# Kernel tuning notes

Hardware: AMD Instinct MI355X
Metric: run time of the kernel (lower is better)

The kernel has to match this reference:

```python
import jax, jax.numpy as jnp
import numpy as np

B, H, S, W, F = 16, 4, 8, 256, 16


def setup_inputs() -> dict:
    key = jax.random.key(0)
    kx, kk = jax.random.split(key)
    x = jax.random.normal(kx, (B, S, W, F), dtype=jnp.float32)
    kernel = jax.random.normal(kk, (H, S, S, W), dtype=jnp.float32)
    return {"x": x, "kernel": kernel}


def reference(x, kernel):
    # kernel: [H, S, S, W]; x: [B, S, W, F]
    Hh, Ss, _, Ww = kernel.shape
    r = jnp.arange(Ww)
    # stacked[h,x,y,j,i] = roll(kernel, shifts=j+1)[i] = kernel[(i-(j+1)) % W]
    idx = (r[None, :] - (r[:, None] + 1)) % Ww          # [W(row=j), W(col=i)]
    stacked = kernel[..., idx]                            # [H,S,S,W,W]
    # torch.tril over last two dims: keep col i <= row j
    tri = (r[None, :] <= r[:, None])                      # [W,W]
    stacked = jnp.where(tri, stacked, jnp.zeros((), dtype=stacked.dtype))
    # masked triangular time-mix contraction
    out = jnp.einsum('hxyji,bxif->bhxyjf', stacked, x)    # [B,H,S,S,W,F]
    base = jnp.arange(1, Ww + 1, dtype=out.dtype).reshape(1, 1, 1, 1, Ww, 1)
    out = out / base
    # transform_x: on diagonal series (x==y) roll time dim by 1, zero first step
    diag_mod = jnp.roll(out, 1, axis=4)
    not_first = (r != 0).reshape(1, 1, 1, 1, Ww, 1)
    diag_mod = diag_mod * not_first.astype(out.dtype)
    eye = jnp.eye(Ss, dtype=bool).reshape(1, 1, Ss, Ss, 1, 1)
    return jnp.where(eye, diag_mod, out)
```

## Files before the change

kernel.cpp:

```cpp
#include <hip/hip_runtime.h>
#include <hip/hip_bf16.h>

typedef short short8 __attribute__((ext_vector_type(8)));
typedef float f32x4 __attribute__((ext_vector_type(4)));

union FragAB { int i[4]; short8 v; };

constexpr int Wc = 256, Fc = 16, Hc = 4, Sc = 8;

__global__ __launch_bounds__(256)
void k_fused(const float* __restrict__ x,
             const float* __restrict__ kern,
             float* __restrict__ out)
{
    __shared__ __align__(16) ushort Xts[128 * 264];
    __shared__ float wext2[2][576];
    __shared__ float rtab[2][256];

    const int blk = blockIdx.x;
    const int c  = blk & 15;
    const int nt = (blk >> 4) & 1;
    const int mt = (blk >> 5) & 1;
    const int sx = blk >> 6;
    const int t = threadIdx.x;

    rtab[0][t] = 1.0f / (float)(t + 1);
    rtab[1][t] = (t > 0) ? 1.0f / (float)t : 0.0f;

    #pragma unroll
    for (int e2 = 0; e2 < 2; ++e2) {
        int hy = c * 2 + e2;
        int h = hy >> 3, sy = hy & 7;
        const float* krow = kern + ((h * Sc + sx) * Sc + sy) * Wc;
        #pragma unroll
        for (int q = 0; q < 3; ++q) {
            int idx = q * 256 + t;
            if (idx < 576) wext2[e2][idx] = (idx >= 320) ? krow[575 - idx] : 0.0f;
        }
    }

    {
        const float4* xbase = reinterpret_cast<const float4*>(x);
        const int b0 = nt * 8;
        #pragma unroll
        for (int it = 0; it < 16; ++it) {
            int id = it * 256 + t;
            int fq = id & 3;
            int k2 = (id >> 2) & 127;
            int bl = id >> 9;
            const float4* rowp = xbase + ((size_t)((b0 + bl) * 8 + sx)) * 1024;
            float4 a = rowp[(2 * k2) * 4 + fq];
            float4 cq = rowp[(2 * k2 + 1) * 4 + fq];
            #pragma unroll
            for (int e = 0; e < 4; ++e) {
                float va = (&a.x)[e], vb = (&cq.x)[e];
                __hip_bfloat16 ha = __float2bfloat16(va);
                __hip_bfloat16 hb = __float2bfloat16(vb);
                uint u = (uint)reinterpret_cast<ushort&>(ha) |
                         ((uint)reinterpret_cast<ushort&>(hb) << 16);
                int row = bl * 16 + fq * 4 + e;
                *reinterpret_cast<uint*>(reinterpret_cast<char*>(Xts) + row * 528 + k2 * 4) = u;
            }
        }
    }
    __syncthreads();

    const int lane = t & 63, wid = t >> 6;
    const int wr = wid >> 1, wc = wid & 1;
    const int wm0 = mt * 128 + wr * 64;
    const int laneM = lane & 15, laneG = lane >> 4;

    const char* bbase = reinterpret_cast<const char*>(Xts) + (wc * 64 + laneM) * 528 + laneG * 16;
    const int kmax = (wm0 + 64 < 256) ? (wm0 + 64) : 256;

    #pragma unroll
    for (int e2 = 0; e2 < 2; ++e2) {
        int hy = c * 2 + e2;
        int h = hy >> 3, sy = hy & 7;
        const int diag = (sx == sy) ? 1 : 0;
        const float* wextf = wext2[e2];
        const float* rt = rtab[diag];
        const int abase = (320 - diag) + wm0 + laneM - 8 * laneG;

        f32x4 zero = {0.0f, 0.0f, 0.0f, 0.0f};
        f32x4 acc[4][4];
        #pragma unroll
        for (int m = 0; m < 4; ++m)
            #pragma unroll
            for (int n = 0; n < 4; ++n) acc[m][n] = zero;

        for (int kc = 0; kc < kmax; kc += 32) {
            FragAB bf[4];
            #pragma unroll
            for (int n = 0; n < 4; ++n) {
                int4 raw = *reinterpret_cast<const int4*>(bbase + n * (16 * 528) + kc * 2);
                bf[n].i[0] = raw.x; bf[n].i[1] = raw.y; bf[n].i[2] = raw.z; bf[n].i[3] = raw.w;
            }
            FragAB af[4];
            #pragma unroll
            for (int m = 0; m < 4; ++m) {
                int idx0 = abase + 16 * m - kc;
                float v[8];
                #pragma unroll
                for (int e = 0; e < 8; ++e) v[e] = wextf[idx0 - e];
                #pragma unroll
                for (int r = 0; r < 4; ++r)
                    af[m].i[r] = (int)__builtin_amdgcn_perm(__float_as_uint(v[2 * r + 1]),
                                                            __float_as_uint(v[2 * r]),
                                                            0x07060302u);
            }
            #pragma unroll
            for (int m = 0; m < 4; ++m)
                #pragma unroll
                for (int n = 0; n < 4; ++n)
                    acc[m][n] = __builtin_amdgcn_mfma_f32_16x16x32_bf16(af[m].v, bf[n].v,
                                                                        acc[m][n], 0, 0, 0);
        }

        #pragma unroll
        for (int n = 0; n < 4; ++n) {
            int b_ = nt * 8 + wc * 4 + n;
            float* ob = out + ((((((size_t)b_ * Hc + h) * Sc + sx) * Sc + sy) * Wc)) * Fc + laneM;
            #pragma unroll
            for (int m = 0; m < 4; ++m) {
                int jb = wm0 + 16 * m + laneG * 4;
                #pragma unroll
                for (int r = 0; r < 4; ++r) {
                    int j = jb + r;
                    ob[(size_t)j * 16] = acc[m][n][r] * rt[j];
                }
            }
        }
    }
}

extern "C" void kernel_launch(void* const* d_in, const int* in_sizes, int n_in,
                              void* d_out, int out_size, void* d_ws, size_t ws_size,
                              hipStream_t stream) {
    const float* x    = (const float*)d_in[0];
    const float* kern = (const float*)d_in[1];
    float* out = (float*)d_out;

    k_fused<<<512, 256, 0, stream>>>(x, kern, out);
}
```

Measured before the change: 24.23 us.

## Swap MFMA operand roles, pre-shift bf16 Toeplitz tables, share X fragments across heads

New measurement: 24.54 us. About the same (+1.3%).

```diff
diff --git a/kernel.cpp b/kernel.cpp
--- a/kernel.cpp
+++ b/kernel.cpp
@@ -4,18 +4,15 @@
 typedef short short8 __attribute__((ext_vector_type(8)));
 typedef float f32x4 __attribute__((ext_vector_type(4)));
 
-union FragAB { int i[4]; short8 v; };
+union FragAB { unsigned long long l[2]; int i[4]; short8 v; };
 
-constexpr int Wc = 256, Fc = 16, Hc = 4, Sc = 8;
-
-__global__ __launch_bounds__(256)
+__global__ __launch_bounds__(256, 2)
 void k_fused(const float* __restrict__ x,
              const float* __restrict__ kern,
              float* __restrict__ out)
 {
     __shared__ __align__(16) ushort Xts[128 * 264];
-    __shared__ float wext2[2][576];
-    __shared__ float rtab[2][256];
+    __shared__ __align__(8)  ushort wforL[2][4][336];
 
     const int blk = blockIdx.x;
     const int c  = blk & 15;
@@ -24,18 +21,23 @@
     const int sx = blk >> 6;
     const int t = threadIdx.x;
 
-    rtab[0][t] = 1.0f / (float)(t + 1);
-    rtab[1][t] = (t > 0) ? 1.0f / (float)t : 0.0f;
-
     #pragma unroll
     for (int e2 = 0; e2 < 2; ++e2) {
-        int hy = c * 2 + e2;
-        int h = hy >> 3, sy = hy & 7;
-        const float* krow = kern + ((h * Sc + sx) * Sc + sy) * Wc;
+        const int hy = c * 2 + e2;
+        const int h = hy >> 3, sy = hy & 7;
+        const float* krow = kern + ((h * 8 + sx) * 8 + sy) * 256;
         #pragma unroll
-        for (int q = 0; q < 3; ++q) {
-            int idx = q * 256 + t;
-            if (idx < 576) wext2[e2][idx] = (idx >= 320) ? krow[575 - idx] : 0.0f;
+        for (int s = 0; s < 4; ++s) {
+            #pragma unroll
+            for (int pass = 0; pass < 2; ++pass) {
+                int q = t + pass * 256;
+                if (q < 336) {
+                    int src = q - s;
+                    float v = (src >= 0 && src < 256) ? krow[src] : 0.0f;
+                    __hip_bfloat16 hv = __float2bfloat16(v);
+                    wforL[e2][s][q] = reinterpret_cast<ushort&>(hv);
+                }
+            }
         }
     }
 
@@ -66,69 +68,84 @@
     __syncthreads();
 
     const int lane = t & 63, wid = t >> 6;
-    const int wr = wid >> 1, wc = wid & 1;
-    const int wm0 = mt * 128 + wr * 64;
+    const int wp = wid >> 1, wj = wid & 1;
     const int laneM = lane & 15, laneG = lane >> 4;
+    const int wj0 = mt * 128 + wj * 64;
+    const int kmax = wj0 + 64;
 
-    const char* bbase = reinterpret_cast<const char*>(Xts) + (wc * 64 + laneM) * 528 + laneG * 16;
-    const int kmax = (wm0 + 64 < 256) ? (wm0 + 64) : 256;
+    const char* XtsB = reinterpret_cast<const char*>(Xts);
+    const char* WB = reinterpret_cast<const char*>(wforL);
+    const int abyte = (wp * 64 + laneM) * 528 + laneG * 16;
 
+    int bB[2];
+    int diagv[2];
     #pragma unroll
     for (int e2 = 0; e2 < 2; ++e2) {
-        int hy = c * 2 + e2;
-        int h = hy >> 3, sy = hy & 7;
+        const int hy = c * 2 + e2;
+        const int sy = hy & 7;
         const int diag = (sx == sy) ? 1 : 0;
-        const float* wextf = wext2[e2];
-        const float* rt = rtab[diag];
-        const int abase = (320 - diag) + wm0 + laneM - 8 * laneG;
+        diagv[e2] = diag;
+        const int w00 = 255 + diag - wj0 - laneM + 8 * laneG;
+        const int s = (laneM - diag + 1) & 3;
+        bB[e2] = e2 * 2688 + s * 674 + 2 * w00;
+    }
 
-        f32x4 zero = {0.0f, 0.0f, 0.0f, 0.0f};
-        f32x4 acc[4][4];
+    f32x4 acc[2][4][4];
+    #pragma unroll
+    for (int e2 = 0; e2 < 2; ++e2)
         #pragma unroll
         for (int m = 0; m < 4; ++m)
             #pragma unroll
-            for (int n = 0; n < 4; ++n) acc[m][n] = zero;
+            for (int n = 0; n < 4; ++n)
+                acc[e2][m][n] = (f32x4){0.0f, 0.0f, 0.0f, 0.0f};
 
-        for (int kc = 0; kc < kmax; kc += 32) {
+    for (int kc = 0; kc < kmax; kc += 32) {
+        FragAB af[4];
+        #pragma unroll
+        for (int m = 0; m < 4; ++m) {
+            const int4 raw = *reinterpret_cast<const int4*>(XtsB + abyte + m * 8448 + kc * 2);
+            af[m].i[0] = raw.x; af[m].i[1] = raw.y;
+            af[m].i[2] = raw.z; af[m].i[3] = raw.w;
+        }
+        #pragma unroll
+        for (int e2 = 0; e2 < 2; ++e2) {
             FragAB bf[4];
             #pragma unroll
             for (int n = 0; n < 4; ++n) {
-                int4 raw = *reinterpret_cast<const int4*>(bbase + n * (16 * 528) + kc * 2);
-                bf[n].i[0] = raw.x; bf[n].i[1] = raw.y; bf[n].i[2] = raw.z; bf[n].i[3] = raw.w;
-            }
-            FragAB af[4];
-            #pragma unroll
-            for (int m = 0; m < 4; ++m) {
-                int idx0 = abase + 16 * m - kc;
-                float v[8];
-                #pragma unroll
-                for (int e = 0; e < 8; ++e) v[e] = wextf[idx0 - e];
-                #pragma unroll
-                for (int r = 0; r < 4; ++r)
-                    af[m].i[r] = (int)__builtin_amdgcn_perm(__float_as_uint(v[2 * r + 1]),
-                                                            __float_as_uint(v[2 * r]),
-                                                            0x07060302u);
+                const char* p = WB + bB[e2] + kc * 2 - 32 * n;
+                bf[n].l[0] = *reinterpret_cast<const unsigned long long*>(p);
+                bf[n].l[1] = *reinterpret_cast<const unsigned long long*>(p + 8);
             }
             #pragma unroll
             for (int m = 0; m < 4; ++m)
                 #pragma unroll
                 for (int n = 0; n < 4; ++n)
-                    acc[m][n] = __builtin_amdgcn_mfma_f32_16x16x32_bf16(af[m].v, bf[n].v,
-                                                                        acc[m][n], 0, 0, 0);
+                    acc[e2][m][n] = __builtin_amdgcn_mfma_f32_16x16x32_bf16(
+                        af[m].v, bf[n].v, acc[e2][m][n], 0, 0, 0);
         }
+    }
 
+    #pragma unroll
+    for (int e2 = 0; e2 < 2; ++e2) {
+        const int hy = c * 2 + e2;
+        const int h = hy >> 3, sy = hy & 7;
+        const int diag = diagv[e2];
         #pragma unroll
         for (int n = 0; n < 4; ++n) {
-            int b_ = nt * 8 + wc * 4 + n;
-            float* ob = out + ((((((size_t)b_ * Hc + h) * Sc + sx) * Sc + sy) * Wc)) * Fc + laneM;
+            const int j = wj0 + 16 * n + laneM;
+            const int denom = j + 1 - diag;
+            const float rt = (denom > 0) ? (1.0f / (float)denom) : 0.0f;
             #pragma unroll
             for (int m = 0; m < 4; ++m) {
-                int jb = wm0 + 16 * m + laneG * 4;
-                #pragma unroll
-                for (int r = 0; r < 4; ++r) {
-                    int j = jb + r;
-                    ob[(size_t)j * 16] = acc[m][n][r] * rt[j];
-                }
+                const int b_ = nt * 8 + wp * 4 + m;
+                float* dst = out + ((((size_t)(b_ * 4 + h) * 8 + sx) * 8 + sy) * 256 + j) * 16
+                             + laneG * 4;
+                float4 v;
+                v.x = acc[e2][m][n][0] * rt;
+                v.y = acc[e2][m][n][1] * rt;
+                v.z = acc[e2][m][n][2] * rt;
+                v.w = acc[e2][m][n][3] * rt;
+                *reinterpret_cast<float4*>(dst) = v;
             }
         }
     }
```
